# Optimization experiments

Hardware: AMD Instinct MI355X
Metric: run time of the kernel (lower is better)

Reference implementation:

```python
import jax, jax.numpy as jnp
import numpy as np

N_NODES = 50000
N_EDGES = 800000
IN_CH = 64
HID = 64
HID2 = HID // 2  # 32


def _sage_conv(x, src, dst, w_l, w_r, b, n_nodes):
    """PyG SAGEConv (aggr='mean', root_weight=True):
    out = lin_l(mean_{j in N(i)} x_j) + lin_r(x_i), bias in lin_l.
    Messages flow src -> dst (source_to_target)."""
    msg = x[src]  # [E, d] gather of source features
    summed = jax.ops.segment_sum(msg, dst, num_segments=n_nodes)  # [N, d]
    cnt = jax.ops.segment_sum(jnp.ones((src.shape[0],), x.dtype), dst,
                              num_segments=n_nodes)  # [N]
    mean = summed / jnp.maximum(cnt, 1.0)[:, None]
    return mean @ w_l + b + x @ w_r


def setup_inputs() -> dict:
    key = jax.random.key(0)
    ks = jax.random.split(key, 12)
    s = 0.05
    x = jax.random.normal(ks[0], (N_NODES, IN_CH), dtype=jnp.float32)
    edge_index = jax.random.randint(ks[1], (2, N_EDGES), 0, N_NODES, dtype=jnp.int32)
    return {
        "x": x,
        "edge_index": edge_index,
        # SAGEConv layer 1 (in -> hidden)
        "w1_l": jax.random.normal(ks[2], (IN_CH, HID), dtype=jnp.float32) * s,
        "w1_r": jax.random.normal(ks[3], (IN_CH, HID), dtype=jnp.float32) * s,
        "b1": jnp.zeros((HID,), jnp.float32),
        # SAGEConv layer 2 (hidden -> hidden//2)
        "w2_l": jax.random.normal(ks[4], (HID, HID2), dtype=jnp.float32) * s,
        "w2_r": jax.random.normal(ks[5], (HID, HID2), dtype=jnp.float32) * s,
        "b2": jnp.zeros((HID2,), jnp.float32),
        # classifier MLP: Linear(32,16) -> ReLU -> Linear(16,2)
        "wc1": jax.random.normal(ks[6], (HID2, 16), dtype=jnp.float32) * s,
        "bc1": jnp.zeros((16,), jnp.float32),
        "wc2": jax.random.normal(ks[7], (16, 2), dtype=jnp.float32) * s,
        "bc2": jnp.zeros((2,), jnp.float32),
    }


def reference(x, edge_index, w1_l, w1_r, b1, w2_l, w2_r, b2, wc1, bc1, wc2, bc2):
    src, dst = edge_index[0], edge_index[1]
    n = x.shape[0]
    # Dropout is identity in eval / deterministic reference.
    h = jax.nn.relu(_sage_conv(x, src, dst, w1_l, w1_r, b1, n))
    h = jax.nn.relu(_sage_conv(h, src, dst, w2_l, w2_r, b2, n))
    h = jax.nn.relu(h @ wc1 + bc1)
    out = h @ wc2 + bc2  # [N, 2]
    return out
```

## Files before the change

kernel.cpp:

```cpp
#include <hip/hip_runtime.h>
#include <hip/hip_fp16.h>

#define N_NODES 50000
#define N_EDGES 800000
#define NBINS   391
#define CAP     4096
#define EPB     4096
#define NBLK_E  ((N_EDGES + EPB - 1) / EPB)
#define NTILE   391
#define LSTRIDE 129

__global__ void k_binA(const int* __restrict__ src, const int* __restrict__ dst,
                       int* __restrict__ bincur, int* __restrict__ binned) {
    __shared__ int cnt[NBINS];
    __shared__ int sc[512];
    __shared__ int lpos[NBINS];
    __shared__ int base[NBINS];
    __shared__ int stage[EPB];
    __shared__ unsigned short sbin[EPB];
    int t = threadIdx.x;
    int blkbase = blockIdx.x * EPB;
    int nE = min(EPB, N_EDGES - blkbase);
    for (int i = t; i < NBINS; i += 256) cnt[i] = 0;
    __syncthreads();
    int sv[16], dv[16];
#pragma unroll
    for (int k = 0; k < 16; ++k) {
        int e = blkbase + t + k * 256;
        if (e < N_EDGES) {
            sv[k] = src[e];
            dv[k] = dst[e];
            atomicAdd(&cnt[dv[k] >> 7], 1);
        } else dv[k] = -1;
    }
    __syncthreads();
    sc[t]       = (t < NBINS) ? cnt[t] : 0;
    sc[t + 256] = (t + 256 < NBINS) ? cnt[t + 256] : 0;
    __syncthreads();
    for (int d = 1; d < 512; d <<= 1) {
        int s0 = t, s1 = t + 256;
        int n0 = sc[s0] + ((s0 >= d) ? sc[s0 - d] : 0);
        int n1 = sc[s1] + ((s1 >= d) ? sc[s1 - d] : 0);
        __syncthreads();
        sc[s0] = n0; sc[s1] = n1;
        __syncthreads();
    }
    for (int b = t; b < NBINS; b += 256) {
        int excl = sc[b] - cnt[b];
        lpos[b] = excl;
        sc[b] = excl;
        if (cnt[b] > 0) base[b] = b * CAP + atomicAdd(&bincur[b], cnt[b]);
    }
    __syncthreads();
#pragma unroll
    for (int k = 0; k < 16; ++k) {
        if (dv[k] >= 0) {
            int b = dv[k] >> 7;
            int p = atomicAdd(&lpos[b], 1);
            stage[p] = (sv[k] & 0xFFFF) | ((dv[k] & 127) << 16);
            sbin[p] = (unsigned short)b;
        }
    }
    __syncthreads();
    for (int i = t; i < nE; i += 256) {
        int b = sbin[i];
        int pos = base[b] + (i - sc[b]);
        if (pos < (b + 1) * CAP) binned[pos] = stage[i];
    }
}

__global__ __launch_bounds__(512) void k_binB_pre1(
        const int* __restrict__ bincur, int* __restrict__ binned,
        int* __restrict__ off, unsigned short* __restrict__ deg,
        int* __restrict__ esrc,
        const float* __restrict__ x,
        const float* __restrict__ wl, const float* __restrict__ wr,
        const float* __restrict__ b,
        __half* __restrict__ ph, float* __restrict__ q) {
    __shared__ float smem[64 * LSTRIDE];
    int t = threadIdx.x;
    int bb = blockIdx.x;
    if (bb < NBINS) {
        int* buf = (int*)smem;
        int* cnt = buf + CAP;
        int* tmp = cnt + 128;
        int* cur = tmp + 128;
        int n0 = bb << 7;
        int seg0 = bb * CAP;
        int n = min(bincur[bb], CAP);
        if (t < 128) cnt[t] = 0;
        __syncthreads();
        for (int i = t; i < n; i += 512) atomicAdd(&cnt[binned[seg0 + i] >> 16], 1);
        __syncthreads();
        int v = (t < 128) ? cnt[t] : 0;
        if (t < 128) tmp[t] = v;
        __syncthreads();
        int val = v;
        for (int d = 1; d < 128; d <<= 1) {
            int add = (t >= d && t < 128) ? tmp[t - d] : 0;
            __syncthreads();
            if (t < 128) { val += add; tmp[t] = val; }
            __syncthreads();
        }
        if (t < 128) {
            int excl = val - v;
            cur[t] = excl;
            int node = n0 + t;
            if (node < N_NODES) {
                off[node] = seg0 + excl;
                deg[node] = (unsigned short)v;
            }
        }
        __syncthreads();
        for (int i = t; i < n; i += 512) {
            int w = binned[seg0 + i];
            int p = atomicAdd(&cur[w >> 16], 1);
            buf[p] = w & 0xFFFF;
        }
        __syncthreads();
        for (int i = t; i < n; i += 512) esrc[seg0 + i] = buf[i];
        return;
    }
    float* sx = smem;
    int g0 = (bb - NBINS) * 128;
#pragma unroll
    for (int i = 0; i < 4; ++i) {
        int f = t + i * 512;
        int nd = f >> 4, cq = f & 15;
        int gn = g0 + nd;
        float4 v = (gn < N_NODES) ? ((const float4*)x)[(size_t)gn * 16 + cq]
                                  : make_float4(0.f, 0.f, 0.f, 0.f);
        sx[(cq * 4 + 0) * LSTRIDE + nd] = v.x;
        sx[(cq * 4 + 1) * LSTRIDE + nd] = v.y;
        sx[(cq * 4 + 2) * LSTRIDE + nd] = v.z;
        sx[(cq * 4 + 3) * LSTRIDE + nd] = v.w;
    }
    __syncthreads();
    int role = __builtin_amdgcn_readfirstlane(t >> 7);
    int wsel = role >> 1;
    int c0 = (role & 1) * 32;
    int ln = t & 127;
    int node = g0 + ln;
    const float* __restrict__ wm = wsel ? wr : wl;
    float acc[32];
    if (wsel) {
#pragma unroll
        for (int c = 0; c < 32; ++c) acc[c] = b[c0 + c];
    } else {
#pragma unroll
        for (int c = 0; c < 32; ++c) acc[c] = 0.f;
    }
#pragma unroll
    for (int k = 0; k < 64; ++k) {
        float xk = sx[k * LSTRIDE + ln];
#pragma unroll
        for (int c = 0; c < 32; ++c)
            acc[c] = fmaf(xk, wm[k * 64 + c0 + c], acc[c]);
    }
    if (node >= N_NODES) return;
    if (wsel == 0) {
        alignas(16) __half2 hv[16];
#pragma unroll
        for (int i = 0; i < 16; ++i)
            hv[i] = __floats2half2_rn(acc[2 * i], acc[2 * i + 1]);
        float4* op = (float4*)(ph + (size_t)node * 64 + c0);
#pragma unroll
        for (int i = 0; i < 4; ++i) op[i] = ((float4*)hv)[i];
    } else {
        float4* op = (float4*)(q + (size_t)node * 64 + c0);
#pragma unroll
        for (int i = 0; i < 8; ++i)
            op[i] = make_float4(acc[4 * i], acc[4 * i + 1], acc[4 * i + 2], acc[4 * i + 3]);
    }
}

__device__ __forceinline__ void acc8(float* a, float4 rv) {
    const __half2* hp = (const __half2*)&rv;
    float2 f0 = __half22float2(hp[0]), f1 = __half22float2(hp[1]);
    float2 f2 = __half22float2(hp[2]), f3 = __half22float2(hp[3]);
    a[0] += f0.x; a[1] += f0.y; a[2] += f1.x; a[3] += f1.y;
    a[4] += f2.x; a[5] += f2.y; a[6] += f3.x; a[7] += f3.y;
}

__global__ __launch_bounds__(256) void k_agg1(const int* __restrict__ off,
                                              const unsigned short* __restrict__ deg,
                                              const int* __restrict__ esrc,
                                              const __half* __restrict__ ph,
                                              const float* __restrict__ q,
                                              float* __restrict__ h1) {
    int wv = threadIdx.x >> 6, lane = threadIdx.x & 63;
    int h = lane >> 5, l32 = lane & 31;
    int node = blockIdx.x * 8 + wv * 2 + h;
    int eg = l32 >> 3;
    int cg = l32 & 7;
    int s0 = off[node];
    int dv = deg[node];
    int s1 = s0 + dv;
    float a0[8] = {0,0,0,0,0,0,0,0}, a1[8] = {0,0,0,0,0,0,0,0};
    float a2[8] = {0,0,0,0,0,0,0,0}, a3[8] = {0,0,0,0,0,0,0,0};
    for (int i = s0; i < s1; i += 16) {
        int i0 = i + eg, i1 = i + 4 + eg, i2 = i + 8 + eg, i3 = i + 12 + eg;
        if (i0 < s1) acc8(a0, *(const float4*)(ph + (size_t)esrc[i0] * 64 + (cg << 3)));
        if (i1 < s1) acc8(a1, *(const float4*)(ph + (size_t)esrc[i1] * 64 + (cg << 3)));
        if (i2 < s1) acc8(a2, *(const float4*)(ph + (size_t)esrc[i2] * 64 + (cg << 3)));
        if (i3 < s1) acc8(a3, *(const float4*)(ph + (size_t)esrc[i3] * 64 + (cg << 3)));
    }
#pragma unroll
    for (int j = 0; j < 8; ++j) a0[j] += a1[j] + (a2[j] + a3[j]);
#pragma unroll
    for (int j = 0; j < 8; ++j) {
        a0[j] += __shfl_xor(a0[j], 8);
        a0[j] += __shfl_xor(a0[j], 16);
    }
    if (eg == 0) {
        float inv = 1.0f / fmaxf((float)dv, 1.0f);
        const float4* qp = (const float4*)(q + (size_t)node * 64 + (cg << 3));
        float4 q0 = qp[0], q1 = qp[1];
        float4 o0, o1;
        o0.x = fmaxf(fmaf(a0[0], inv, q0.x), 0.f);
        o0.y = fmaxf(fmaf(a0[1], inv, q0.y), 0.f);
        o0.z = fmaxf(fmaf(a0[2], inv, q0.z), 0.f);
        o0.w = fmaxf(fmaf(a0[3], inv, q0.w), 0.f);
        o1.x = fmaxf(fmaf(a0[4], inv, q1.x), 0.f);
        o1.y = fmaxf(fmaf(a0[5], inv, q1.y), 0.f);
        o1.z = fmaxf(fmaf(a0[6], inv, q1.z), 0.f);
        o1.w = fmaxf(fmaf(a0[7], inv, q1.w), 0.f);
        float4* op = (float4*)(h1 + (size_t)node * 64 + (cg << 3));
        op[0] = o0; op[1] = o1;
    }
}

__global__ __launch_bounds__(256) void k_pre2(const float* __restrict__ h1,
                                              const float* __restrict__ w2l,
                                              const float* __restrict__ w2r,
                                              const float* __restrict__ b2,
                                              __half* __restrict__ zh,
                                              float* __restrict__ r) {
    __shared__ float sx[64 * LSTRIDE];
    int t = threadIdx.x;
    int g0 = blockIdx.x * 128;
#pragma unroll
    for (int i = 0; i < 8; ++i) {
        int f = t + i * 256;
        int nd = f >> 4, cq = f & 15;
        int gn = g0 + nd;
        float4 v = (gn < N_NODES) ? ((const float4*)h1)[(size_t)gn * 16 + cq]
                                  : make_float4(0.f, 0.f, 0.f, 0.f);
        sx[(cq * 4 + 0) * LSTRIDE + nd] = v.x;
        sx[(cq * 4 + 1) * LSTRIDE + nd] = v.y;
        sx[(cq * 4 + 2) * LSTRIDE + nd] = v.z;
        sx[(cq * 4 + 3) * LSTRIDE + nd] = v.w;
    }
    __syncthreads();
    int role = __builtin_amdgcn_readfirstlane(t >> 7);
    int ln = t & 127;
    int node = g0 + ln;
    const float* __restrict__ wm = role ? w2r : w2l;
    float acc[32];
    if (role) {
#pragma unroll
        for (int c = 0; c < 32; ++c) acc[c] = b2[c];
    } else {
#pragma unroll
        for (int c = 0; c < 32; ++c) acc[c] = 0.f;
    }
#pragma unroll
    for (int k = 0; k < 64; ++k) {
        float xk = sx[k * LSTRIDE + ln];
#pragma unroll
        for (int c = 0; c < 32; ++c)
            acc[c] = fmaf(xk, wm[k * 32 + c], acc[c]);
    }
    if (node >= N_NODES) return;
    if (role == 0) {
        alignas(16) __half2 hv[16];
#pragma unroll
        for (int i = 0; i < 16; ++i)
            hv[i] = __floats2half2_rn(acc[2 * i], acc[2 * i + 1]);
        float4* op = (float4*)(zh + (size_t)node * 32);
#pragma unroll
        for (int i = 0; i < 4; ++i) op[i] = ((float4*)hv)[i];
    } else {
        float4* op = (float4*)(r + (size_t)node * 32);
#pragma unroll
        for (int i = 0; i < 8; ++i)
            op[i] = make_float4(acc[4 * i], acc[4 * i + 1], acc[4 * i + 2], acc[4 * i + 3]);
    }
}

__global__ __launch_bounds__(256) void k_agg2cls(const int* __restrict__ off,
                                                 const unsigned short* __restrict__ deg,
                                                 const int* __restrict__ esrc,
                                                 const __half* __restrict__ zh,
                                                 const float* __restrict__ r,
                                                 const float* __restrict__ wc1,
                                                 const float* __restrict__ bc1,
                                                 const float* __restrict__ wc2,
                                                 const float* __restrict__ bc2,
                                                 float* __restrict__ out) {
    __shared__ float sh2[16 * 33];
    __shared__ float sh3[16 * 17];
    __shared__ float swc1[512];
    __shared__ float sbc1[16];
    __shared__ float swc2[32];
    __shared__ float sbc2[2];
    int t = threadIdx.x;
    swc1[t] = wc1[t];
    swc1[t + 256] = wc1[t + 256];
    if (t < 16) sbc1[t] = bc1[t];
    if (t < 32) swc2[t] = wc2[t];
    if (t < 2)  sbc2[t] = bc2[t];

    int lane = t & 63;
    int l16 = lane & 15;
    int nl = (t >> 4) & 15;
    int node = blockIdx.x * 16 + nl;
    int eg = l16 >> 2;
    int cg = l16 & 3;
    int s0 = off[node];
    int dv = deg[node];
    int s1 = s0 + dv;
    float a0[8] = {0,0,0,0,0,0,0,0}, a1[8] = {0,0,0,0,0,0,0,0};
    float a2[8] = {0,0,0,0,0,0,0,0}, a3[8] = {0,0,0,0,0,0,0,0};
    for (int i = s0; i < s1; i += 16) {
        int i0 = i + eg, i1 = i + 4 + eg, i2 = i + 8 + eg, i3 = i + 12 + eg;
        if (i0 < s1) acc8(a0, *(const float4*)(zh + (size_t)esrc[i0] * 32 + (cg << 3)));
        if (i1 < s1) acc8(a1, *(const float4*)(zh + (size_t)esrc[i1] * 32 + (cg << 3)));
        if (i2 < s1) acc8(a2, *(const float4*)(zh + (size_t)esrc[i2] * 32 + (cg << 3)));
        if (i3 < s1) acc8(a3, *(const float4*)(zh + (size_t)esrc[i3] * 32 + (cg << 3)));
    }
#pragma unroll
    for (int j = 0; j < 8; ++j) a0[j] += a1[j] + (a2[j] + a3[j]);
#pragma unroll
    for (int j = 0; j < 8; ++j) {
        a0[j] += __shfl_xor(a0[j], 4);
        a0[j] += __shfl_xor(a0[j], 8);
    }
    if (eg == 0) {
        float inv = 1.0f / fmaxf((float)dv, 1.0f);
        const float4* rp = (const float4*)(r + (size_t)node * 32 + (cg << 3));
        float4 r0 = rp[0], r1 = rp[1];
        float* d = sh2 + nl * 33 + (cg << 3);
        d[0] = fmaxf(fmaf(a0[0], inv, r0.x), 0.f);
        d[1] = fmaxf(fmaf(a0[1], inv, r0.y), 0.f);
        d[2] = fmaxf(fmaf(a0[2], inv, r0.z), 0.f);
        d[3] = fmaxf(fmaf(a0[3], inv, r0.w), 0.f);
        d[4] = fmaxf(fmaf(a0[4], inv, r1.x), 0.f);
        d[5] = fmaxf(fmaf(a0[5], inv, r1.y), 0.f);
        d[6] = fmaxf(fmaf(a0[6], inv, r1.z), 0.f);
        d[7] = fmaxf(fmaf(a0[7], inv, r1.w), 0.f);
    }
    __syncthreads();
    int n = t >> 4, j = t & 15;
    float acc1 = sbc1[j];
#pragma unroll
    for (int k = 0; k < 32; ++k)
        acc1 = fmaf(sh2[n * 33 + k], swc1[k * 16 + j], acc1);
    sh3[n * 17 + j] = fmaxf(acc1, 0.f);
    __syncthreads();
    if (t < 16) {
        int nn = t;
        float o0 = sbc2[0], o1 = sbc2[1];
#pragma unroll
        for (int k = 0; k < 16; ++k) {
            float h3k = sh3[nn * 17 + k];
            o0 = fmaf(h3k, swc2[k * 2 + 0], o0);
            o1 = fmaf(h3k, swc2[k * 2 + 1], o1);
        }
        int gnode = blockIdx.x * 16 + nn;
        *(float2*)(out + (size_t)gnode * 2) = make_float2(o0, o1);
    }
}

extern "C" void kernel_launch(void* const* d_in, const int* in_sizes, int n_in,
                              void* d_out, int out_size, void* d_ws, size_t ws_size,
                              hipStream_t stream) {
    const float* x   = (const float*)d_in[0];
    const int*   ei  = (const int*)d_in[1];
    const int*   src = ei;
    const int*   dst = ei + N_EDGES;
    const float* w1l = (const float*)d_in[2];
    const float* w1r = (const float*)d_in[3];
    const float* b1  = (const float*)d_in[4];
    const float* w2l = (const float*)d_in[5];
    const float* w2r = (const float*)d_in[6];
    const float* b2  = (const float*)d_in[7];
    const float* wc1 = (const float*)d_in[8];
    const float* bc1 = (const float*)d_in[9];
    const float* wc2 = (const float*)d_in[10];
    const float* bc2 = (const float*)d_in[11];
    float* out = (float*)d_out;

    int*   wi     = (int*)d_ws;
    int*   bincur = wi;
    int*   binned = wi + 400;
    int*   esrc   = binned + (size_t)NBINS * CAP;
    int*   off    = esrc + (size_t)NBINS * CAP;
    unsigned short* deg = (unsigned short*)(off + N_NODES);
    float* h1     = (float*)(deg + N_NODES + (N_NODES & 1));
    float* q      = h1 + (size_t)64 * N_NODES;
    float* phf    = q + (size_t)64 * N_NODES;
    __half* ph    = (__half*)phf;
    __half* zh    = (__half*)q;
    float*  r     = q + (size_t)16 * N_NODES;

    hipMemsetAsync(bincur, 0, 400 * sizeof(int), stream);
    k_binA<<<NBLK_E, 256, 0, stream>>>(src, dst, bincur, binned);

    k_binB_pre1<<<NBINS + NTILE, 512, 0, stream>>>(bincur, binned, off, deg, esrc,
                                                   x, w1l, w1r, b1, ph, q);

    k_agg1<<<N_NODES / 8, 256, 0, stream>>>(off, deg, esrc, ph, q, h1);

    k_pre2<<<NTILE, 256, 0, stream>>>(h1, w2l, w2r, b2, zh, r);
    k_agg2cls<<<N_NODES / 16, 256, 0, stream>>>(off, deg, esrc, zh, r,
                                                wc1, bc1, wc2, bc2, out);
}
```

Measured before the change: 186.5 us.

## Fuse layer-1 aggregation with layer-2 projection and widen binning blocks

Merges the layer-1 mean-aggregation kernel with the layer-2 linear projection. Each 1024-thread block aggregates 128 nodes into shared memory and then runs the 64x32 matmuls on them, which removes the h1 round trip through global memory and one kernel launch. The matmul is split across 8 thread groups by role and output-column slice. The binning kernel also moves from 256 to 512 threads per block. The trade-off is fewer, larger blocks (391) for the aggregation, which may reduce latency hiding for the irregular gather, and a serialized transition between the two phases inside each block.

```diff
diff --git a/kernel.cpp b/kernel.cpp
--- a/kernel.cpp
+++ b/kernel.cpp
@@ -10,8 +10,10 @@
 #define NTILE   391
 #define LSTRIDE 129
 
-__global__ void k_binA(const int* __restrict__ src, const int* __restrict__ dst,
-                       int* __restrict__ bincur, int* __restrict__ binned) {
+__global__ __launch_bounds__(512) void k_binA(const int* __restrict__ src,
+                                              const int* __restrict__ dst,
+                                              int* __restrict__ bincur,
+                                              int* __restrict__ binned) {
     __shared__ int cnt[NBINS];
     __shared__ int sc[512];
     __shared__ int lpos[NBINS];
@@ -21,12 +23,12 @@
     int t = threadIdx.x;
     int blkbase = blockIdx.x * EPB;
     int nE = min(EPB, N_EDGES - blkbase);
-    for (int i = t; i < NBINS; i += 256) cnt[i] = 0;
-    __syncthreads();
-    int sv[16], dv[16];
-#pragma unroll
-    for (int k = 0; k < 16; ++k) {
-        int e = blkbase + t + k * 256;
+    for (int i = t; i < NBINS; i += 512) cnt[i] = 0;
+    __syncthreads();
+    int sv[8], dv[8];
+#pragma unroll
+    for (int k = 0; k < 8; ++k) {
+        int e = blkbase + t + k * 512;
         if (e < N_EDGES) {
             sv[k] = src[e];
             dv[k] = dst[e];
@@ -34,18 +36,15 @@
         } else dv[k] = -1;
     }
     __syncthreads();
-    sc[t]       = (t < NBINS) ? cnt[t] : 0;
-    sc[t + 256] = (t + 256 < NBINS) ? cnt[t + 256] : 0;
+    sc[t] = (t < NBINS) ? cnt[t] : 0;
     __syncthreads();
     for (int d = 1; d < 512; d <<= 1) {
-        int s0 = t, s1 = t + 256;
-        int n0 = sc[s0] + ((s0 >= d) ? sc[s0 - d] : 0);
-        int n1 = sc[s1] + ((s1 >= d) ? sc[s1 - d] : 0);
-        __syncthreads();
-        sc[s0] = n0; sc[s1] = n1;
-        __syncthreads();
-    }
-    for (int b = t; b < NBINS; b += 256) {
+        int add = (t >= d) ? sc[t - d] : 0;
+        __syncthreads();
+        sc[t] += add;
+        __syncthreads();
+    }
+    for (int b = t; b < NBINS; b += 512) {
         int excl = sc[b] - cnt[b];
         lpos[b] = excl;
         sc[b] = excl;
@@ -53,7 +52,7 @@
     }
     __syncthreads();
 #pragma unroll
-    for (int k = 0; k < 16; ++k) {
+    for (int k = 0; k < 8; ++k) {
         if (dv[k] >= 0) {
             int b = dv[k] >> 7;
             int p = atomicAdd(&lpos[b], 1);
@@ -62,7 +61,7 @@
         }
     }
     __syncthreads();
-    for (int i = t; i < nE; i += 256) {
+    for (int i = t; i < nE; i += 512) {
         int b = sbin[i];
         int pos = base[b] + (i - sc[b]);
         if (pos < (b + 1) * CAP) binned[pos] = stage[i];
@@ -182,109 +181,92 @@
     a[4] += f2.x; a[5] += f2.y; a[6] += f3.x; a[7] += f3.y;
 }
 
-__global__ __launch_bounds__(256) void k_agg1(const int* __restrict__ off,
-                                              const unsigned short* __restrict__ deg,
-                                              const int* __restrict__ esrc,
-                                              const __half* __restrict__ ph,
-                                              const float* __restrict__ q,
-                                              float* __restrict__ h1) {
-    int wv = threadIdx.x >> 6, lane = threadIdx.x & 63;
-    int h = lane >> 5, l32 = lane & 31;
-    int node = blockIdx.x * 8 + wv * 2 + h;
+__global__ __launch_bounds__(1024) void k_agg1_pre2(
+        const int* __restrict__ off, const unsigned short* __restrict__ deg,
+        const int* __restrict__ esrc,
+        const __half* __restrict__ ph, const float* __restrict__ q,
+        const float* __restrict__ w2l, const float* __restrict__ w2r,
+        const float* __restrict__ b2,
+        __half* __restrict__ zh, float* __restrict__ r) {
+    __shared__ float sx[64 * LSTRIDE];
+    int t = threadIdx.x;
+    int n0 = blockIdx.x << 7;
+    int half = t >> 5;
+    int l32 = t & 31;
     int eg = l32 >> 3;
     int cg = l32 & 7;
-    int s0 = off[node];
-    int dv = deg[node];
-    int s1 = s0 + dv;
-    float a0[8] = {0,0,0,0,0,0,0,0}, a1[8] = {0,0,0,0,0,0,0,0};
-    float a2[8] = {0,0,0,0,0,0,0,0}, a3[8] = {0,0,0,0,0,0,0,0};
-    for (int i = s0; i < s1; i += 16) {
-        int i0 = i + eg, i1 = i + 4 + eg, i2 = i + 8 + eg, i3 = i + 12 + eg;
-        if (i0 < s1) acc8(a0, *(const float4*)(ph + (size_t)esrc[i0] * 64 + (cg << 3)));
-        if (i1 < s1) acc8(a1, *(const float4*)(ph + (size_t)esrc[i1] * 64 + (cg << 3)));
-        if (i2 < s1) acc8(a2, *(const float4*)(ph + (size_t)esrc[i2] * 64 + (cg << 3)));
-        if (i3 < s1) acc8(a3, *(const float4*)(ph + (size_t)esrc[i3] * 64 + (cg << 3)));
-    }
-#pragma unroll
-    for (int j = 0; j < 8; ++j) a0[j] += a1[j] + (a2[j] + a3[j]);
-#pragma unroll
-    for (int j = 0; j < 8; ++j) {
-        a0[j] += __shfl_xor(a0[j], 8);
-        a0[j] += __shfl_xor(a0[j], 16);
-    }
-    if (eg == 0) {
-        float inv = 1.0f / fmaxf((float)dv, 1.0f);
-        const float4* qp = (const float4*)(q + (size_t)node * 64 + (cg << 3));
-        float4 q0 = qp[0], q1 = qp[1];
-        float4 o0, o1;
-        o0.x = fmaxf(fmaf(a0[0], inv, q0.x), 0.f);
-        o0.y = fmaxf(fmaf(a0[1], inv, q0.y), 0.f);
-        o0.z = fmaxf(fmaf(a0[2], inv, q0.z), 0.f);
-        o0.w = fmaxf(fmaf(a0[3], inv, q0.w), 0.f);
-        o1.x = fmaxf(fmaf(a0[4], inv, q1.x), 0.f);
-        o1.y = fmaxf(fmaf(a0[5], inv, q1.y), 0.f);
-        o1.z = fmaxf(fmaf(a0[6], inv, q1.z), 0.f);
-        o1.w = fmaxf(fmaf(a0[7], inv, q1.w), 0.f);
-        float4* op = (float4*)(h1 + (size_t)node * 64 + (cg << 3));
-        op[0] = o0; op[1] = o1;
-    }
-}
-
-__global__ __launch_bounds__(256) void k_pre2(const float* __restrict__ h1,
-                                              const float* __restrict__ w2l,
-                                              const float* __restrict__ w2r,
-                                              const float* __restrict__ b2,
-                                              __half* __restrict__ zh,
-                                              float* __restrict__ r) {
-    __shared__ float sx[64 * LSTRIDE];
-    int t = threadIdx.x;
-    int g0 = blockIdx.x * 128;
-#pragma unroll
-    for (int i = 0; i < 8; ++i) {
-        int f = t + i * 256;
-        int nd = f >> 4, cq = f & 15;
-        int gn = g0 + nd;
-        float4 v = (gn < N_NODES) ? ((const float4*)h1)[(size_t)gn * 16 + cq]
-                                  : make_float4(0.f, 0.f, 0.f, 0.f);
-        sx[(cq * 4 + 0) * LSTRIDE + nd] = v.x;
-        sx[(cq * 4 + 1) * LSTRIDE + nd] = v.y;
-        sx[(cq * 4 + 2) * LSTRIDE + nd] = v.z;
-        sx[(cq * 4 + 3) * LSTRIDE + nd] = v.w;
-    }
-    __syncthreads();
-    int role = __builtin_amdgcn_readfirstlane(t >> 7);
+    for (int p = 0; p < 4; ++p) {
+        int nl = half + 32 * p;
+        int node = n0 + nl;
+        if (node < N_NODES) {
+            int s0 = off[node];
+            int dv = deg[node];
+            int s1 = s0 + dv;
+            float a0[8] = {0,0,0,0,0,0,0,0}, a1[8] = {0,0,0,0,0,0,0,0};
+            float a2[8] = {0,0,0,0,0,0,0,0}, a3[8] = {0,0,0,0,0,0,0,0};
+            for (int i = s0; i < s1; i += 16) {
+                int i0 = i + eg, i1 = i + 4 + eg, i2 = i + 8 + eg, i3 = i + 12 + eg;
+                if (i0 < s1) acc8(a0, *(const float4*)(ph + (size_t)esrc[i0] * 64 + (cg << 3)));
+                if (i1 < s1) acc8(a1, *(const float4*)(ph + (size_t)esrc[i1] * 64 + (cg << 3)));
+                if (i2 < s1) acc8(a2, *(const float4*)(ph + (size_t)esrc[i2] * 64 + (cg << 3)));
+                if (i3 < s1) acc8(a3, *(const float4*)(ph + (size_t)esrc[i3] * 64 + (cg << 3)));
+            }
+#pragma unroll
+            for (int j = 0; j < 8; ++j) a0[j] += a1[j] + (a2[j] + a3[j]);
+#pragma unroll
+            for (int j = 0; j < 8; ++j) {
+                a0[j] += __shfl_xor(a0[j], 8);
+                a0[j] += __shfl_xor(a0[j], 16);
+            }
+            if (eg == 0) {
+                float inv = 1.0f / fmaxf((float)dv, 1.0f);
+                const float4* qp = (const float4*)(q + (size_t)node * 64 + (cg << 3));
+                float4 q0 = qp[0], q1 = qp[1];
+                float* d = sx + (cg << 3) * LSTRIDE + nl;
+                d[0 * LSTRIDE] = fmaxf(fmaf(a0[0], inv, q0.x), 0.f);
+                d[1 * LSTRIDE] = fmaxf(fmaf(a0[1], inv, q0.y), 0.f);
+                d[2 * LSTRIDE] = fmaxf(fmaf(a0[2], inv, q0.z), 0.f);
+                d[3 * LSTRIDE] = fmaxf(fmaf(a0[3], inv, q0.w), 0.f);
+                d[4 * LSTRIDE] = fmaxf(fmaf(a0[4], inv, q1.x), 0.f);
+                d[5 * LSTRIDE] = fmaxf(fmaf(a0[5], inv, q1.y), 0.f);
+                d[6 * LSTRIDE] = fmaxf(fmaf(a0[6], inv, q1.z), 0.f);
+                d[7 * LSTRIDE] = fmaxf(fmaf(a0[7], inv, q1.w), 0.f);
+            }
+        }
+    }
+    __syncthreads();
+    int g = __builtin_amdgcn_readfirstlane(t >> 7);
+    int role = g & 1;
+    int c0 = (g >> 1) * 8;
     int ln = t & 127;
-    int node = g0 + ln;
+    int node = n0 + ln;
     const float* __restrict__ wm = role ? w2r : w2l;
-    float acc[32];
+    float acc[8];
     if (role) {
 #pragma unroll
-        for (int c = 0; c < 32; ++c) acc[c] = b2[c];
+        for (int c = 0; c < 8; ++c) acc[c] = b2[c0 + c];
     } else {
 #pragma unroll
-        for (int c = 0; c < 32; ++c) acc[c] = 0.f;
+        for (int c = 0; c < 8; ++c) acc[c] = 0.f;
     }
 #pragma unroll
     for (int k = 0; k < 64; ++k) {
         float xk = sx[k * LSTRIDE + ln];
 #pragma unroll
-        for (int c = 0; c < 32; ++c)
-            acc[c] = fmaf(xk, wm[k * 32 + c], acc[c]);
+        for (int c = 0; c < 8; ++c)
+            acc[c] = fmaf(xk, wm[k * 32 + c0 + c], acc[c]);
     }
     if (node >= N_NODES) return;
     if (role == 0) {
-        alignas(16) __half2 hv[16];
-#pragma unroll
-        for (int i = 0; i < 16; ++i)
+        alignas(16) __half2 hv[4];
+#pragma unroll
+        for (int i = 0; i < 4; ++i)
             hv[i] = __floats2half2_rn(acc[2 * i], acc[2 * i + 1]);
-        float4* op = (float4*)(zh + (size_t)node * 32);
-#pragma unroll
-        for (int i = 0; i < 4; ++i) op[i] = ((float4*)hv)[i];
+        *(float4*)(zh + (size_t)node * 32 + c0) = *(float4*)hv;
     } else {
-        float4* op = (float4*)(r + (size_t)node * 32);
-#pragma unroll
-        for (int i = 0; i < 8; ++i)
-            op[i] = make_float4(acc[4 * i], acc[4 * i + 1], acc[4 * i + 2], acc[4 * i + 3]);
+        float4* op = (float4*)(r + (size_t)node * 32 + c0);
+        op[0] = make_float4(acc[0], acc[1], acc[2], acc[3]);
+        op[1] = make_float4(acc[4], acc[5], acc[6], acc[7]);
     }
 }
 
@@ -397,22 +379,22 @@
     int*   esrc   = binned + (size_t)NBINS * CAP;
     int*   off    = esrc + (size_t)NBINS * CAP;
     unsigned short* deg = (unsigned short*)(off + N_NODES);
-    float* h1     = (float*)(deg + N_NODES + (N_NODES & 1));
-    float* q      = h1 + (size_t)64 * N_NODES;
+    float* q      = (float*)(deg + N_NODES + (N_NODES & 1));
     float* phf    = q + (size_t)64 * N_NODES;
     __half* ph    = (__half*)phf;
-    __half* zh    = (__half*)q;
-    float*  r     = q + (size_t)16 * N_NODES;
+    float* zhf    = phf + (size_t)32 * N_NODES;
+    __half* zh    = (__half*)zhf;
+    float* r      = zhf + (size_t)16 * N_NODES;
 
     hipMemsetAsync(bincur, 0, 400 * sizeof(int), stream);
-    k_binA<<<NBLK_E, 256, 0, stream>>>(src, dst, bincur, binned);
+    k_binA<<<NBLK_E, 512, 0, stream>>>(src, dst, bincur, binned);
 
     k_binB_pre1<<<NBINS + NTILE, 512, 0, stream>>>(bincur, binned, off, deg, esrc,
                                                    x, w1l, w1r, b1, ph, q);
 
-    k_agg1<<<N_NODES / 8, 256, 0, stream>>>(off, deg, esrc, ph, q, h1);
-
-    k_pre2<<<NTILE, 256, 0, stream>>>(h1, w2l, w2r, b2, zh, r);
+    k_agg1_pre2<<<NBINS, 1024, 0, stream>>>(off, deg, esrc, ph, q,
+                                            w2l, w2r, b2, zh, r);
+
     k_agg2cls<<<N_NODES / 16, 256, 0, stream>>>(off, deg, esrc, zh, r,
                                                 wc1, bc1, wc2, bc2, out);
 }
```

Measured after the change: 187.5 us, median of 2. No clear change (+0.5%).
